# Optimization experiments

Hardware: AMD Instinct MI355X
Metric: run time of the kernel (lower is better)

The kernel has to match this reference:

```python
import jax, jax.numpy as jnp
import numpy as np

DIM = 1024
HEADS = 16
HEAD_DIM = DIM // HEADS
DFF = 4 * DIM  # SwiGLU expansion=4.0
EPS = 1e-5
NEG = -1e4  # original uses -1e4 causal mask, not -inf


def rms_norm(x, w):
    v = jnp.mean(x * x, axis=-1, keepdims=True)
    return w * (x * jax.lax.rsqrt(v + EPS))


def rotate_half(x):
    x1, x2 = jnp.split(x, 2, axis=-1)
    return jnp.concatenate((-x2, x1), axis=-1)


def setup_inputs() -> dict:
    key = jax.random.key(0)
    ks = jax.random.split(key, 12)
    B, S = 2, 2048
    s = 0.02
    h = jax.random.normal(ks[0], (B, S, DIM), jnp.float32)
    # RoPE tables, half-split convention: emb = concat(freqs, freqs)
    inv_freq = 1.0 / (10000.0 ** (np.arange(0, HEAD_DIM, 2, dtype=np.float32) / HEAD_DIM))
    freqs = np.arange(S, dtype=np.float32)[:, None] * inv_freq[None, :]
    emb = np.concatenate([freqs, freqs], axis=-1)
    cos = jnp.asarray(np.cos(emb))  # [S, HEAD_DIM]
    sin = jnp.asarray(np.sin(emb))
    return {
        "h": h, "cos": cos, "sin": sin,
        "norm1_w": jnp.ones((DIM,), jnp.float32),
        "wq": jax.random.normal(ks[1], (DIM, DIM), jnp.float32) * s,
        "wk": jax.random.normal(ks[2], (DIM, DIM), jnp.float32) * s,
        "wv": jax.random.normal(ks[3], (DIM, DIM), jnp.float32) * s,
        "wo": jax.random.normal(ks[4], (DIM, DIM), jnp.float32) * s,
        "norm2_w": jnp.ones((DIM,), jnp.float32),
        "gate_w": jax.random.normal(ks[5], (DFF, DIM), jnp.float32) * s,
        "gate_b": jnp.zeros((DFF,), jnp.float32),
        "up_w": jax.random.normal(ks[6], (DFF, DIM), jnp.float32) * s,
        "up_b": jnp.zeros((DFF,), jnp.float32),
        "down_w": jax.random.normal(ks[7], (DIM, DFF), jnp.float32) * s,
        "down_b": jnp.zeros((DIM,), jnp.float32),
        "gate": jnp.full((DIM,), 0.5, jnp.float32),
    }


def reference(h, cos, sin, norm1_w, wq, wk, wv, wo, norm2_w,
              gate_w, gate_b, up_w, up_b, down_w, down_b, gate):
    B, S, _ = h.shape
    scale = HEAD_DIM ** -0.5

    x = rms_norm(h, norm1_w)

    def heads(t):  # [B,S,DIM] -> [B,H,S,D]
        return t.reshape(B, S, HEADS, HEAD_DIM).transpose(0, 2, 1, 3)

    q = heads(x @ wq.T)
    k = heads(x @ wk.T)
    v = heads(x @ wv.T)

    # inline RoPE (cos/sin broadcast [S,D] over [B,H,S,D])
    q = q * cos + rotate_half(q) * sin
    k = k * cos + rotate_half(k) * sin

    scores = jnp.einsum('bhsd,bhtd->bhst', q, k) * scale
    causal = jnp.triu(jnp.full((S, S), NEG, jnp.float32), k=1)
    scores = scores + causal
    attn = jax.nn.softmax(scores, axis=-1)
    out = jnp.einsum('bhst,bhtd->bhsd', attn, v)
    out = out.transpose(0, 2, 1, 3).reshape(B, S, DIM)
    attn_out = out @ wo.T

    h = h + attn_out

    x2 = rms_norm(h, norm2_w)
    g = jax.nn.silu(x2 @ gate_w.T + gate_b)
    u = x2 @ up_w.T + up_b
    mlp = (g * u) @ down_w.T + down_b

    h = h + jax.nn.sigmoid(gate) * mlp
    return h
```

## Files before the change

kernel.cpp:

```cpp
#include <hip/hip_runtime.h>
#include <math.h>

#define DIM    1024
#define HEADS  16
#define HD     64
#define SEQ    2048
#define BATCH  2
#define TTOK   4096
#define DFF    4096
#define S3     3072

typedef __attribute__((ext_vector_type(8))) short short8;
typedef __attribute__((ext_vector_type(4))) float f32x4;

__device__ __forceinline__ float bf2f(unsigned short u) {
  union { unsigned int u; float f; } v; v.u = ((unsigned int)u) << 16; return v.f;
}
__device__ __forceinline__ unsigned short f2bf(float f) {
  union { float f; unsigned int u; } v; v.f = f;
  return (unsigned short)((v.u + 0x7FFFu + ((v.u >> 16) & 1u)) >> 16);
}
__device__ __forceinline__ unsigned short f2bf_trunc(float f) {
  union { float f; unsigned int u; } v; v.f = f;
  return (unsigned short)(v.u >> 16);
}

#define AS1(p) ((const __attribute__((address_space(1))) void*)(p))
#define AS3(p) ((__attribute__((address_space(3))) void*)(p))

__global__ __launch_bounds__(256) void conv4_k(
    const float* __restrict__ src, unsigned short* __restrict__ dst, int n4)
{
  const int i = blockIdx.x * 256 + threadIdx.x;
  if (i >= n4) return;
  const float4 f = ((const float4*)src)[i];
  unsigned long long o = (unsigned long long)f2bf(f.x)
                       | ((unsigned long long)f2bf(f.y) << 16)
                       | ((unsigned long long)f2bf(f.z) << 32)
                       | ((unsigned long long)f2bf(f.w) << 48);
  ((unsigned long long*)dst)[i] = o;
}

template<int MODE>
__global__ __launch_bounds__(256) void gemm_bt(
    const unsigned short* __restrict__ A,
    const unsigned short* __restrict__ W,
    unsigned short* __restrict__ C,
    float* __restrict__ Cf,
    const float* __restrict__ bias,
    const float* __restrict__ resf,
    const float* __restrict__ gate,
    const float* __restrict__ cosp,
    const float* __restrict__ sinp,
    int M, int N, int K)
{
  __shared__ __align__(16) unsigned short As[128 * 64];
  __shared__ __align__(16) unsigned short Bs[128 * 64];

  const int tid  = threadIdx.x;
  const int lane = tid & 63;
  const int wv   = tid >> 6;
  const int row0 = blockIdx.x * 128;
  const int col0 = blockIdx.y * 128;
  const int wm   = (wv >> 1) * 64;
  const int wn   = (wv & 1) * 64;
  const int lr   = lane & 15;
  const int lg   = lane >> 4;

  const int srow = lane >> 3;
  const int skg  = (lane & 7) ^ srow;

  f32x4 acc[4][4];
#pragma unroll
  for (int i = 0; i < 4; i++)
#pragma unroll
    for (int j = 0; j < 4; j++) acc[i][j] = (f32x4){0.f, 0.f, 0.f, 0.f};

  for (int k0 = 0; k0 < K; k0 += 64) {
#pragma unroll
    for (int i = 0; i < 4; i++) {
      const int c = wv * 4 + i;
      const unsigned short* ga = A + (size_t)(row0 + c * 8 + srow) * K + k0 + skg * 8;
      __builtin_amdgcn_global_load_lds(AS1(ga), AS3(As + c * 512), 16, 0, 0);
      const unsigned short* gb = W + (size_t)(col0 + c * 8 + srow) * K + k0 + skg * 8;
      __builtin_amdgcn_global_load_lds(AS1(gb), AS3(Bs + c * 512), 16, 0, 0);
    }
    __syncthreads();

#pragma unroll
    for (int ks = 0; ks < 2; ks++) {
      short8 af[4], bf[4];
#pragma unroll
      for (int i = 0; i < 4; i++) {
        const int r = wm + i * 16 + lr;
        af[i] = *(const short8*)(As + r * 64 + (((ks * 4 + lg) ^ (lr & 7)) * 8));
      }
#pragma unroll
      for (int j = 0; j < 4; j++) {
        const int r = wn + j * 16 + lr;
        bf[j] = *(const short8*)(Bs + r * 64 + (((ks * 4 + lg) ^ (lr & 7)) * 8));
      }
#pragma unroll
      for (int i = 0; i < 4; i++)
#pragma unroll
        for (int j = 0; j < 4; j++)
          acc[i][j] = __builtin_amdgcn_mfma_f32_16x16x32_bf16(af[i], bf[j], acc[i][j], 0, 0, 0);
    }
    __syncthreads();
  }

  if (MODE == 5) {
    const bool do_rope = (col0 < 2048);
#pragma unroll
    for (int i = 0; i < 4; i++) {
#pragma unroll
      for (int r = 0; r < 4; r++) {
        const int row = row0 + wm + i * 16 + lg * 4 + r;
        const int s = row & (SEQ - 1);
        const size_t rb = (size_t)row * N + col0 + wn;
        if (do_rope) {
#pragma unroll
          for (int jp = 0; jp < 2; jp++) {
            const int d = jp * 16 + lr;
            const float c = cosp[s * HD + d];
            const float sn = sinp[s * HD + d];
            const float x1v = acc[i][jp][r];
            const float x2v = acc[i][jp + 2][r];
            C[rb + d]      = f2bf(x1v * c - x2v * sn);
            C[rb + d + 32] = f2bf(x2v * c + x1v * sn);
          }
        } else {
#pragma unroll
          for (int j = 0; j < 4; j++)
            C[rb + j * 16 + lr] = f2bf(acc[i][j][r]);
        }
      }
    }
    return;
  }

#pragma unroll
  for (int i = 0; i < 4; i++) {
#pragma unroll
    for (int j = 0; j < 4; j++) {
      const int col = col0 + wn + j * 16 + lr;
#pragma unroll
      for (int r = 0; r < 4; r++) {
        const int row = row0 + wm + i * 16 + lg * 4 + r;
        float v = acc[i][j][r];
        const size_t idx = (size_t)row * N + col;
        if (MODE == 3) {
          Cf[idx] = v + resf[idx];
        } else if (MODE == 4) {
          const float sg = 1.0f / (1.0f + __expf(-gate[col]));
          Cf[idx] = Cf[idx] + sg * (v + bias[col]);
        }
      }
    }
  }
}

__global__ __launch_bounds__(256) void gemm_swiglu(
    const unsigned short* __restrict__ A,
    const unsigned short* __restrict__ Wg,
    const unsigned short* __restrict__ Wu,
    unsigned short* __restrict__ G,
    const float* __restrict__ gb,
    const float* __restrict__ ub,
    int M, int N, int K)
{
  __shared__ __align__(16) unsigned short As[128 * 64];
  __shared__ __align__(16) unsigned short Gs[128 * 64];
  __shared__ __align__(16) unsigned short Us[128 * 64];

  const int tid  = threadIdx.x;
  const int lane = tid & 63;
  const int wv   = tid >> 6;
  const int row0 = blockIdx.x * 128;
  const int col0 = blockIdx.y * 128;
  const int wm   = (wv >> 1) * 64;
  const int wn   = (wv & 1) * 64;
  const int lr   = lane & 15;
  const int lg   = lane >> 4;

  const int srow = lane >> 3;
  const int skg  = (lane & 7) ^ srow;

  f32x4 ag[4][4], au[4][4];
#pragma unroll
  for (int i = 0; i < 4; i++)
#pragma unroll
    for (int j = 0; j < 4; j++) {
      ag[i][j] = (f32x4){0.f, 0.f, 0.f, 0.f};
      au[i][j] = (f32x4){0.f, 0.f, 0.f, 0.f};
    }

  for (int k0 = 0; k0 < K; k0 += 64) {
#pragma unroll
    for (int i = 0; i < 4; i++) {
      const int c = wv * 4 + i;
      const unsigned short* ga = A + (size_t)(row0 + c * 8 + srow) * K + k0 + skg * 8;
      __builtin_amdgcn_global_load_lds(AS1(ga), AS3(As + c * 512), 16, 0, 0);
      const unsigned short* gg = Wg + (size_t)(col0 + c * 8 + srow) * K + k0 + skg * 8;
      __builtin_amdgcn_global_load_lds(AS1(gg), AS3(Gs + c * 512), 16, 0, 0);
      const unsigned short* gu = Wu + (size_t)(col0 + c * 8 + srow) * K + k0 + skg * 8;
      __builtin_amdgcn_global_load_lds(AS1(gu), AS3(Us + c * 512), 16, 0, 0);
    }
    __syncthreads();

#pragma unroll
    for (int ks = 0; ks < 2; ks++) {
      short8 af[4], bg[4], bu[4];
#pragma unroll
      for (int i = 0; i < 4; i++) {
        const int r = wm + i * 16 + lr;
        af[i] = *(const short8*)(As + r * 64 + (((ks * 4 + lg) ^ (lr & 7)) * 8));
      }
#pragma unroll
      for (int j = 0; j < 4; j++) {
        const int r = wn + j * 16 + lr;
        const int off = (((ks * 4 + lg) ^ (lr & 7)) * 8);
        bg[j] = *(const short8*)(Gs + r * 64 + off);
        bu[j] = *(const short8*)(Us + r * 64 + off);
      }
#pragma unroll
      for (int i = 0; i < 4; i++)
#pragma unroll
        for (int j = 0; j < 4; j++) {
          ag[i][j] = __builtin_amdgcn_mfma_f32_16x16x32_bf16(af[i], bg[j], ag[i][j], 0, 0, 0);
          au[i][j] = __builtin_amdgcn_mfma_f32_16x16x32_bf16(af[i], bu[j], au[i][j], 0, 0, 0);
        }
    }
    __syncthreads();
  }

#pragma unroll
  for (int i = 0; i < 4; i++) {
#pragma unroll
    for (int j = 0; j < 4; j++) {
      const int col = col0 + wn + j * 16 + lr;
#pragma unroll
      for (int r = 0; r < 4; r++) {
        const int row = row0 + wm + i * 16 + lg * 4 + r;
        float g = ag[i][j][r] + gb[col];
        g = g / (1.0f + __expf(-g));
        const float u = au[i][j][r] + ub[col];
        G[(size_t)row * N + col] = f2bf(g * u);
      }
    }
  }
}

template<int XF32>
__global__ __launch_bounds__(256) void rmsnorm_k(
    const void* __restrict__ Xv,
    const float* __restrict__ W,
    unsigned short* __restrict__ Y)
{
  const int t  = blockIdx.x;
  const int i0 = threadIdx.x * 4;

  float v[4];
  if (XF32) {
    const float4 f = *(const float4*)((const float*)Xv + (size_t)t * DIM + i0);
    v[0] = f.x; v[1] = f.y; v[2] = f.z; v[3] = f.w;
  } else {
    unsigned long long raw = *(const unsigned long long*)((const unsigned short*)Xv + (size_t)t * DIM + i0);
#pragma unroll
    for (int k = 0; k < 4; k++) v[k] = bf2f((unsigned short)(raw >> (16 * k)));
  }

  float ss = v[0] * v[0] + v[1] * v[1] + v[2] * v[2] + v[3] * v[3];
#pragma unroll
  for (int off = 32; off > 0; off >>= 1) ss += __shfl_xor(ss, off);

  __shared__ float red[4];
  if ((threadIdx.x & 63) == 0) red[threadIdx.x >> 6] = ss;
  __syncthreads();
  const float tot = red[0] + red[1] + red[2] + red[3];
  const float r = rsqrtf(tot * (1.0f / DIM) + 1e-5f);

  const float4 wf = *(const float4*)(W + i0);
  const float wv4[4] = {wf.x, wf.y, wf.z, wf.w};
  unsigned long long o = 0;
#pragma unroll
  for (int k = 0; k < 4; k++)
    o |= ((unsigned long long)f2bf(v[k] * r * wv4[k])) << (16 * k);
  *(unsigned long long*)(Y + (size_t)t * DIM + i0) = o;
}

__device__ const unsigned char cqt[24] = {8,9,10,11,12,13,14,15,7,15,6,14,5,13,4,12,3,11,2,10,1,9,0,8};
__device__ const unsigned char cck[24] = {0,0,0,0,0,0,0,0,0,1,0,1,0,1,0,1,0,1,0,1,0,1,0,1};

__global__ __launch_bounds__(256) void fattn_k(
    const unsigned short* __restrict__ QKV,
    unsigned short* __restrict__ O,
    unsigned short* __restrict__ Pbuf,
    float* __restrict__ Lbuf)
{
  __shared__ __align__(16) unsigned short Ks[64 * 64];
  __shared__ __align__(16) unsigned short Vt[64 * 72];
  __shared__ __align__(16) unsigned short Ps[4 * 32 * 72];

  const int tid  = threadIdx.x;
  const int lane = tid & 63;
  const int wv   = tid >> 6;
  const int lr   = lane & 15;
  const int lg   = lane >> 4;

  const int j  = blockIdx.x;
  const int bh = blockIdx.y;
  const int qt = cqt[j];
  const int ck = cck[j];
  const int b  = bh >> 4, h = bh & 15;
  const int q0 = qt * 128;
  const int c0 = ck * 1024;
  const int kend = min(q0 + 128, c0 + 1024);
  const size_t rowb = (size_t)b * SEQ;
  const int qoff = h * HD;
  const int koff = 1024 + h * HD;
  const int voff = 2048 + h * HD;

  short8 aq[2][2];
#pragma unroll
  for (int rf = 0; rf < 2; rf++) {
    const size_t tok = rowb + q0 + wv * 32 + rf * 16 + lr;
    aq[rf][0] = *(const short8*)(QKV + tok * S3 + qoff + lg * 8);
    aq[rf][1] = *(const short8*)(QKV + tok * S3 + qoff + 32 + lg * 8);
  }

  f32x4 o[2][4];
  f32x4 lacc[2];
#pragma unroll
  for (int rf = 0; rf < 2; rf++) {
    lacc[rf] = (f32x4){0.f, 0.f, 0.f, 0.f};
#pragma unroll
    for (int d = 0; d < 4; d++) o[rf][d] = (f32x4){0.f, 0.f, 0.f, 0.f};
  }
  short8 onesb;
#pragma unroll
  for (int jj = 0; jj < 8; jj++) onesb[jj] = (short)0x3F80;

  const int srow = lane >> 3;
  const int skg  = (lane & 7) ^ srow;
  const int kv   = tid >> 2;
  const int d0   = (tid & 3) * 16;

  const float C1 = 0.125f * 1.44269504f;
  const float C2 = 11.5415603f;

  for (int t0 = c0; t0 < kend; t0 += 64) {
#pragma unroll
    for (int i = 0; i < 2; i++) {
      const int c = wv * 2 + i;
      const unsigned short* gk = QKV + (rowb + t0 + c * 8 + srow) * S3 + koff + skg * 8;
      __builtin_amdgcn_global_load_lds(AS1(gk), AS3(Ks + c * 512), 16, 0, 0);
    }
    {
      const unsigned short* gv = QKV + (rowb + t0 + kv) * S3 + voff + d0;
      const short8 v0 = *(const short8*)gv;
      const short8 v1 = *(const short8*)(gv + 8);
      const int klo = kv & 7, khi = kv >> 3;
#pragma unroll
      for (int w = 0; w < 8; w++) {
        const int da = d0 + w, db2 = d0 + 8 + w;
        Vt[da  * 72 + ((khi ^ ((da  >> 3) & 7)) * 8) + klo] = (unsigned short)v0[w];
        Vt[db2 * 72 + ((khi ^ ((db2 >> 3) & 7)) * 8) + klo] = (unsigned short)v1[w];
      }
    }
    __syncthreads();

    f32x4 S[2][4];
#pragma unroll
    for (int sub = 0; sub < 4; sub++) {
      const int kr = sub * 16 + lr;
      const short8 bk0 = *(const short8*)(Ks + kr * 64 + ((lg       ^ (kr & 7)) * 8));
      const short8 bk1 = *(const short8*)(Ks + kr * 64 + (((4 + lg) ^ (kr & 7)) * 8));
#pragma unroll
      for (int rf = 0; rf < 2; rf++) {
        f32x4 s = (f32x4){0.f, 0.f, 0.f, 0.f};
        s = __builtin_amdgcn_mfma_f32_16x16x32_bf16(aq[rf][0], bk0, s, 0, 0, 0);
        s = __builtin_amdgcn_mfma_f32_16x16x32_bf16(aq[rf][1], bk1, s, 0, 0, 0);
        S[rf][sub] = s;
      }
    }

    unsigned short* pw = Ps + wv * (32 * 72);
#pragma unroll
    for (int rf = 0; rf < 2; rf++) {
      const int qmin = q0 + wv * 32 + rf * 16;
      const bool diag = (t0 + 63 > qmin);
#pragma unroll
      for (int sub = 0; sub < 4; sub++) {
#pragma unroll
        for (int r = 0; r < 4; r++) {
          float t = fmaf(S[rf][sub][r], C1, -C2);
          if (diag && (t0 + sub * 16 + lr > qmin + lg * 4 + r)) t = -INFINITY;
          const float p = exp2f(t);
          pw[(rf * 16 + lg * 4 + r) * 72 + sub * 16 + lr] = f2bf_trunc(p);
        }
      }
    }

#pragma unroll
    for (int kf = 0; kf < 2; kf++) {
      const short8 pa0 = *(const short8*)(pw + lr * 72 + kf * 32 + lg * 8);
      const short8 pa1 = *(const short8*)(pw + (16 + lr) * 72 + kf * 32 + lg * 8);
      lacc[0] = __builtin_amdgcn_mfma_f32_16x16x32_bf16(pa0, onesb, lacc[0], 0, 0, 0);
      lacc[1] = __builtin_amdgcn_mfma_f32_16x16x32_bf16(pa1, onesb, lacc[1], 0, 0, 0);
#pragma unroll
      for (int dsub = 0; dsub < 4; dsub++) {
        const int d = dsub * 16 + lr;
        const short8 bvf = *(const short8*)(Vt + d * 72 +
                             (((kf * 4 + lg) ^ ((d >> 3) & 7)) * 8));
        o[0][dsub] = __builtin_amdgcn_mfma_f32_16x16x32_bf16(pa0, bvf, o[0][dsub], 0, 0, 0);
        o[1][dsub] = __builtin_amdgcn_mfma_f32_16x16x32_bf16(pa1, bvf, o[1][dsub], 0, 0, 0);
      }
    }
    __syncthreads();
  }

  if (qt < 8) {
#pragma unroll
    for (int rf = 0; rf < 2; rf++) {
      float inv[4];
#pragma unroll
      for (int r = 0; r < 4; r++) inv[r] = 1.0f / lacc[rf][r];
#pragma unroll
      for (int dsub = 0; dsub < 4; dsub++)
#pragma unroll
        for (int r = 0; r < 4; r++)
          O[(rowb + q0 + wv * 32 + rf * 16 + lg * 4 + r) * DIM + h * HD + dsub * 16 + lr] =
              f2bf(o[rf][dsub][r] * inv[r]);
    }
  } else {
    const int pidx = (bh * 8 + (qt - 8)) * 2 + ck;
    unsigned short* pb = Pbuf + (size_t)pidx * (128 * 64);
    float* lb = Lbuf + pidx * 128;
#pragma unroll
    for (int rf = 0; rf < 2; rf++) {
      const int rbase = wv * 32 + rf * 16 + lg * 4;
      if (lr == 0) {
#pragma unroll
        for (int r = 0; r < 4; r++) lb[rbase + r] = lacc[rf][r];
      }
#pragma unroll
      for (int dsub = 0; dsub < 4; dsub++)
#pragma unroll
        for (int r = 0; r < 4; r++)
          pb[(rbase + r) * 64 + dsub * 16 + lr] = f2bf(o[rf][dsub][r]);
    }
  }
}

__global__ __launch_bounds__(256) void fattn_combine_k(
    const unsigned short* __restrict__ Pbuf,
    const float* __restrict__ Lbuf,
    unsigned short* __restrict__ O)
{
  const int qt = blockIdx.x + 8;
  const int bh = blockIdx.y;
  const int b  = bh >> 4, h = bh & 15;
  const int q0 = qt * 128;
  const size_t rowb = (size_t)b * SEQ;
  const int p0 = (bh * 8 + blockIdx.x) * 2;

  const unsigned short* pa = Pbuf + (size_t)p0 * (128 * 64);
  const unsigned short* pb = pa + 128 * 64;
  const float* la = Lbuf + p0 * 128;
  const float* lb = la + 128;

#pragma unroll
  for (int it = 0; it < 4; it++) {
    const int idx = it * 2048 + threadIdx.x * 8;
    const int row = idx >> 6;
    const int col = idx & 63;
    const short8 v0 = *(const short8*)(pa + idx);
    const short8 v1 = *(const short8*)(pb + idx);
    const float inv = 1.0f / (la[row] + lb[row]);
    short8 r;
#pragma unroll
    for (int w = 0; w < 8; w++)
      r[w] = (short)f2bf((bf2f((unsigned short)v0[w]) + bf2f((unsigned short)v1[w])) * inv);
    *(short8*)(O + (rowb + q0 + row) * DIM + h * HD + col) = r;
  }
}

extern "C" void kernel_launch(void* const* d_in, const int* in_sizes, int n_in,
                              void* d_out, int out_size, void* d_ws, size_t ws_size,
                              hipStream_t stream)
{
  const float* h    = (const float*)d_in[0];
  const float* cosb = (const float*)d_in[1];
  const float* sinb = (const float*)d_in[2];
  const float* n1w  = (const float*)d_in[3];
  const float* n2w  = (const float*)d_in[8];
  const float* gb   = (const float*)d_in[10];
  const float* ub   = (const float*)d_in[12];
  const float* db   = (const float*)d_in[14];
  const float* gatep= (const float*)d_in[15];
  float* out = (float*)d_out;

  unsigned short* ws = (unsigned short*)d_ws;
  const size_t M1 = 1u << 20;

  unsigned short* wqkv = ws;
  unsigned short* wo_c = ws + 3 * M1;
  unsigned short* gw_c = ws + 4 * M1;
  unsigned short* uw_c = ws + 8 * M1;
  unsigned short* dw_c = ws + 12 * M1;
  unsigned short* x1   = ws + 16 * M1;
  unsigned short* Pbuf = ws + 16 * M1;
  unsigned short* x2   = ws + 16 * M1;
  float*          Lbuf = (float*)ws;
  unsigned short* qkv  = ws + 20 * M1;
  unsigned short* attn = ws + 32 * M1;
  unsigned short* g    = qkv;

  const dim3 blk(256);
  const dim3 gq(TTOK / 128, S3 / 128);
  const dim3 g1(TTOK / 128, DIM / 128);
  const dim3 g2(TTOK / 128, DFF / 128);

  auto cv = [&](int i, unsigned short* dst) {
    const int n4 = in_sizes[i] / 4;
    conv4_k<<<(n4 + 255) / 256, blk, 0, stream>>>((const float*)d_in[i], dst, n4);
  };
  cv(4, wqkv); cv(5, wqkv + M1); cv(6, wqkv + 2 * M1); cv(7, wo_c);
  cv(9, gw_c); cv(11, uw_c); cv(13, dw_c);

  rmsnorm_k<1><<<TTOK, blk, 0, stream>>>(h, n1w, x1);

  gemm_bt<5><<<gq, blk, 0, stream>>>(x1, wqkv, qkv, nullptr, nullptr, nullptr,
                                     nullptr, cosb, sinb, TTOK, S3, DIM);

  fattn_k<<<dim3(24, BATCH * HEADS), blk, 0, stream>>>(qkv, attn, Pbuf, Lbuf);
  fattn_combine_k<<<dim3(8, BATCH * HEADS), blk, 0, stream>>>(Pbuf, Lbuf, attn);

  gemm_bt<3><<<g1, blk, 0, stream>>>(attn, wo_c, nullptr, out, nullptr, h,
                                     nullptr, nullptr, nullptr, TTOK, DIM, DIM);

  rmsnorm_k<1><<<TTOK, blk, 0, stream>>>(out, n2w, x2);

  gemm_swiglu<<<g2, blk, 0, stream>>>(x2, gw_c, uw_c, g, gb, ub, TTOK, DFF, DIM);

  gemm_bt<4><<<g1, blk, 0, stream>>>(g, dw_c, nullptr, out, db, nullptr,
                                     gatep, nullptr, nullptr, TTOK, DIM, DFF);
}
```

Measured before the change: 494.5 us.

## Split-K down projection, rebalance causal attention tiles, merge weight conversions, double-buffer KV

Merges the seven weight-conversion launches into one kernel. The down-projection GEMM becomes a 4-way split-K whose bf16 partials are summed by a new combine kernel that also applies bias, sigmoid gate and residual. Flash attention uses a new 32-block schedule that splits long causal query tiles into up to three chunks for load balance, and double-buffers K/V in shared memory so the next tile loads while the current one computes. The aim is better occupancy on the 256-CU device and less launch overhead. The cost is extra partial-sum traffic, a bf16 rounding of partials, and complex hand-coded schedule tables.

After: 465.1 us. 1.06x faster.

```diff
diff --git a/kernel.cpp b/kernel.cpp
--- a/kernel.cpp
+++ b/kernel.cpp
@@ -28,12 +28,21 @@
 #define AS1(p) ((const __attribute__((address_space(1))) void*)(p))
 #define AS3(p) ((__attribute__((address_space(3))) void*)(p))
 
-__global__ __launch_bounds__(256) void conv4_k(
-    const float* __restrict__ src, unsigned short* __restrict__ dst, int n4)
+__global__ __launch_bounds__(256) void wconv_k(
+    const float* __restrict__ s0, const float* __restrict__ s1,
+    const float* __restrict__ s2, const float* __restrict__ s3,
+    const float* __restrict__ s4, const float* __restrict__ s5,
+    const float* __restrict__ s6, unsigned short* __restrict__ dst)
 {
   const int i = blockIdx.x * 256 + threadIdx.x;
-  if (i >= n4) return;
-  const float4 f = ((const float4*)src)[i];
+  const float* s; int base;
+  if (i < 1048576) {
+    if (i < 524288) { if (i < 262144) { s = s0; base = 0; } else { s = s1; base = 262144; } }
+    else            { if (i < 786432) { s = s2; base = 524288; } else { s = s3; base = 786432; } }
+  } else if (i < 2097152) { s = s4; base = 1048576; }
+  else if (i < 3145728)   { s = s5; base = 2097152; }
+  else                    { s = s6; base = 3145728; }
+  const float4 f = ((const float4*)s)[i - base];
   unsigned long long o = (unsigned long long)f2bf(f.x)
                        | ((unsigned long long)f2bf(f.y) << 16)
                        | ((unsigned long long)f2bf(f.z) << 32)
@@ -47,9 +56,7 @@
     const unsigned short* __restrict__ W,
     unsigned short* __restrict__ C,
     float* __restrict__ Cf,
-    const float* __restrict__ bias,
     const float* __restrict__ resf,
-    const float* __restrict__ gate,
     const float* __restrict__ cosp,
     const float* __restrict__ sinp,
     int M, int N, int K)
@@ -70,13 +77,16 @@
   const int srow = lane >> 3;
   const int skg  = (lane & 7) ^ srow;
 
+  int kb = 0, ke = K;
+  if (MODE == 6) { kb = blockIdx.z * 1024; ke = kb + 1024; }
+
   f32x4 acc[4][4];
 #pragma unroll
   for (int i = 0; i < 4; i++)
 #pragma unroll
     for (int j = 0; j < 4; j++) acc[i][j] = (f32x4){0.f, 0.f, 0.f, 0.f};
 
-  for (int k0 = 0; k0 < K; k0 += 64) {
+  for (int k0 = kb; k0 < ke; k0 += 64) {
 #pragma unroll
     for (int i = 0; i < 4; i++) {
       const int c = wv * 4 + i;
@@ -139,6 +149,11 @@
     return;
   }
 
+  unsigned short* Cz = C;
+  if (MODE == 6) {
+    const size_t pz[4] = {4u * 1048576u, 8u * 1048576u, 16u * 1048576u, 0u};
+    Cz = C + pz[blockIdx.z];
+  }
 #pragma unroll
   for (int i = 0; i < 4; i++) {
 #pragma unroll
@@ -147,17 +162,42 @@
 #pragma unroll
       for (int r = 0; r < 4; r++) {
         const int row = row0 + wm + i * 16 + lg * 4 + r;
-        float v = acc[i][j][r];
+        const float v = acc[i][j][r];
         const size_t idx = (size_t)row * N + col;
         if (MODE == 3) {
           Cf[idx] = v + resf[idx];
-        } else if (MODE == 4) {
-          const float sg = 1.0f / (1.0f + __expf(-gate[col]));
-          Cf[idx] = Cf[idx] + sg * (v + bias[col]);
+        } else if (MODE == 6) {
+          Cz[idx] = f2bf(v);
         }
       }
     }
   }
+}
+
+__global__ __launch_bounds__(256) void dcomb_k(
+    const unsigned short* __restrict__ ws, float* __restrict__ out,
+    const float* __restrict__ db, const float* __restrict__ gate)
+{
+  const int i4 = blockIdx.x * 256 + threadIdx.x;
+  const size_t idx = (size_t)i4 * 4;
+  const int col = (int)(idx & 1023);
+  const unsigned long long p0 = *(const unsigned long long*)(ws + 4u * 1048576u + idx);
+  const unsigned long long p1 = *(const unsigned long long*)(ws + 8u * 1048576u + idx);
+  const unsigned long long p2 = *(const unsigned long long*)(ws + 16u * 1048576u + idx);
+  const unsigned long long p3 = *(const unsigned long long*)(ws + idx);
+  float4 o = *(float4*)(out + idx);
+  float* op = (float*)&o;
+#pragma unroll
+  for (int w = 0; w < 4; w++) {
+    const float s = bf2f((unsigned short)(p0 >> (16 * w)))
+                  + bf2f((unsigned short)(p1 >> (16 * w)))
+                  + bf2f((unsigned short)(p2 >> (16 * w)))
+                  + bf2f((unsigned short)(p3 >> (16 * w)))
+                  + db[col + w];
+    const float sg = 1.0f / (1.0f + __expf(-gate[col + w]));
+    op[w] += sg * s;
+  }
+  *(float4*)(out + idx) = o;
 }
 
 __global__ __launch_bounds__(256) void gemm_swiglu(
@@ -289,8 +329,11 @@
   *(unsigned long long*)(Y + (size_t)t * DIM + i0) = o;
 }
 
-__device__ const unsigned char cqt[24] = {8,9,10,11,12,13,14,15,7,15,6,14,5,13,4,12,3,11,2,10,1,9,0,8};
-__device__ const unsigned char cck[24] = {0,0,0,0,0,0,0,0,0,1,0,1,0,1,0,1,0,1,0,1,0,1,0,1};
+__device__ const unsigned char cqt[32] = {10,10,15,15,9,9,13,14,14,14,15,4,8,8,12,12,13,13,7,7,11,11,11,12,3,6,6,5,5,2,1,0};
+__device__ const unsigned char ctb[32] = {0,11,0,11,0,10,0,0,10,20,22,0,0,9,0,9,10,19,0,8,0,8,16,18,0,0,7,0,6,0,0,0};
+__device__ const unsigned char ccnt[32] = {11,11,11,11,10,10,10,10,10,10,10,10,9,9,9,9,9,9,8,8,8,8,8,8,8,7,7,6,6,6,4,2};
+__device__ const unsigned char cchv[32] = {0,1,0,1,0,1,0,0,1,2,2,0,0,1,0,1,1,2,0,1,0,1,2,2,0,0,1,0,1,0,0,0};
+__device__ const unsigned char cpsv[32] = {255,5,255,14,255,4,255,255,12,13,15,255,255,3,255,8,10,11,255,2,255,6,7,9,255,255,1,255,0,255,255,255};
 
 __global__ __launch_bounds__(256) void fattn_k(
     const unsigned short* __restrict__ QKV,
@@ -298,8 +341,8 @@
     unsigned short* __restrict__ Pbuf,
     float* __restrict__ Lbuf)
 {
-  __shared__ __align__(16) unsigned short Ks[64 * 64];
-  __shared__ __align__(16) unsigned short Vt[64 * 72];
+  __shared__ __align__(16) unsigned short Ks[2][64 * 64];
+  __shared__ __align__(16) unsigned short Vt[2][64 * 72];
   __shared__ __align__(16) unsigned short Ps[4 * 32 * 72];
 
   const int tid  = threadIdx.x;
@@ -311,15 +354,16 @@
   const int j  = blockIdx.x;
   const int bh = blockIdx.y;
   const int qt = cqt[j];
-  const int ck = cck[j];
+  const int tb = ctb[j];
+  const int nt = ccnt[j];
+  const int ch = cchv[j];
+  const int ps = cpsv[j];
   const int b  = bh >> 4, h = bh & 15;
   const int q0 = qt * 128;
-  const int c0 = ck * 1024;
-  const int kend = min(q0 + 128, c0 + 1024);
   const size_t rowb = (size_t)b * SEQ;
   const int qoff = h * HD;
-  const int koff = 1024 + h * HD;
-  const int voff = 2048 + h * HD;
+  const int koff = 1024 + qoff;
+  const int voff = 2048 + qoff;
 
   short8 aq[2][2];
 #pragma unroll
@@ -349,33 +393,44 @@
   const float C1 = 0.125f * 1.44269504f;
   const float C2 = 11.5415603f;
 
-  for (int t0 = c0; t0 < kend; t0 += 64) {
+  auto stage = [&](int buf, int ti) {
+    const int t0 = (tb + ti) * 64;
+    unsigned short* ksb = &Ks[buf][0];
 #pragma unroll
     for (int i = 0; i < 2; i++) {
       const int c = wv * 2 + i;
       const unsigned short* gk = QKV + (rowb + t0 + c * 8 + srow) * S3 + koff + skg * 8;
-      __builtin_amdgcn_global_load_lds(AS1(gk), AS3(Ks + c * 512), 16, 0, 0);
-    }
-    {
-      const unsigned short* gv = QKV + (rowb + t0 + kv) * S3 + voff + d0;
-      const short8 v0 = *(const short8*)gv;
-      const short8 v1 = *(const short8*)(gv + 8);
-      const int klo = kv & 7, khi = kv >> 3;
-#pragma unroll
-      for (int w = 0; w < 8; w++) {
-        const int da = d0 + w, db2 = d0 + 8 + w;
-        Vt[da  * 72 + ((khi ^ ((da  >> 3) & 7)) * 8) + klo] = (unsigned short)v0[w];
-        Vt[db2 * 72 + ((khi ^ ((db2 >> 3) & 7)) * 8) + klo] = (unsigned short)v1[w];
-      }
-    }
+      __builtin_amdgcn_global_load_lds(AS1(gk), AS3(ksb + c * 512), 16, 0, 0);
+    }
+    unsigned short* vtb = &Vt[buf][0];
+    const unsigned short* gv = QKV + (rowb + t0 + kv) * S3 + voff + d0;
+    const short8 v0 = *(const short8*)gv;
+    const short8 v1 = *(const short8*)(gv + 8);
+    const int klo = kv & 7, khi = kv >> 3;
+#pragma unroll
+    for (int w = 0; w < 8; w++) {
+      const int da = d0 + w, db2 = d0 + 8 + w;
+      vtb[da  * 72 + ((khi ^ ((da  >> 3) & 7)) * 8) + klo] = (unsigned short)v0[w];
+      vtb[db2 * 72 + ((khi ^ ((db2 >> 3) & 7)) * 8) + klo] = (unsigned short)v1[w];
+    }
+  };
+
+  stage(0, 0);
+
+  for (int ti = 0; ti < nt; ti++) {
     __syncthreads();
+    if (ti + 1 < nt) stage((ti + 1) & 1, ti + 1);
+
+    const int t0 = (tb + ti) * 64;
+    const unsigned short* ksb = &Ks[ti & 1][0];
+    const unsigned short* vtb = &Vt[ti & 1][0];
 
     f32x4 S[2][4];
 #pragma unroll
     for (int sub = 0; sub < 4; sub++) {
       const int kr = sub * 16 + lr;
-      const short8 bk0 = *(const short8*)(Ks + kr * 64 + ((lg       ^ (kr & 7)) * 8));
-      const short8 bk1 = *(const short8*)(Ks + kr * 64 + (((4 + lg) ^ (kr & 7)) * 8));
+      const short8 bk0 = *(const short8*)(ksb + kr * 64 + ((lg       ^ (kr & 7)) * 8));
+      const short8 bk1 = *(const short8*)(ksb + kr * 64 + (((4 + lg) ^ (kr & 7)) * 8));
 #pragma unroll
       for (int rf = 0; rf < 2; rf++) {
         f32x4 s = (f32x4){0.f, 0.f, 0.f, 0.f};
@@ -411,16 +466,15 @@
 #pragma unroll
       for (int dsub = 0; dsub < 4; dsub++) {
         const int d = dsub * 16 + lr;
-        const short8 bvf = *(const short8*)(Vt + d * 72 +
+        const short8 bvf = *(const short8*)(vtb + d * 72 +
                              (((kf * 4 + lg) ^ ((d >> 3) & 7)) * 8));
         o[0][dsub] = __builtin_amdgcn_mfma_f32_16x16x32_bf16(pa0, bvf, o[0][dsub], 0, 0, 0);
         o[1][dsub] = __builtin_amdgcn_mfma_f32_16x16x32_bf16(pa1, bvf, o[1][dsub], 0, 0, 0);
       }
     }
-    __syncthreads();
-  }
-
-  if (qt < 8) {
+  }
+
+  if (ps == 255 && qt < 5) {
 #pragma unroll
     for (int rf = 0; rf < 2; rf++) {
       float inv[4];
@@ -434,21 +488,35 @@
               f2bf(o[rf][dsub][r] * inv[r]);
     }
   } else {
-    const int pidx = (bh * 8 + (qt - 8)) * 2 + ck;
-    unsigned short* pb = Pbuf + (size_t)pidx * (128 * 64);
-    float* lb = Lbuf + pidx * 128;
+    const int lbase = ((bh * 11 + (qt - 5)) * 3 + ch) * 128;
 #pragma unroll
     for (int rf = 0; rf < 2; rf++) {
       const int rbase = wv * 32 + rf * 16 + lg * 4;
       if (lr == 0) {
 #pragma unroll
-        for (int r = 0; r < 4; r++) lb[rbase + r] = lacc[rf][r];
-      }
-#pragma unroll
-      for (int dsub = 0; dsub < 4; dsub++)
-#pragma unroll
-        for (int r = 0; r < 4; r++)
-          pb[(rbase + r) * 64 + dsub * 16 + lr] = f2bf(o[rf][dsub][r]);
+        for (int r = 0; r < 4; r++) Lbuf[lbase + rbase + r] = lacc[rf][r];
+      }
+    }
+    if (ps == 255) {
+#pragma unroll
+      for (int rf = 0; rf < 2; rf++)
+#pragma unroll
+        for (int dsub = 0; dsub < 4; dsub++)
+#pragma unroll
+          for (int r = 0; r < 4; r++)
+            O[(rowb + q0 + wv * 32 + rf * 16 + lg * 4 + r) * DIM + h * HD + dsub * 16 + lr] =
+                f2bf(o[rf][dsub][r]);
+    } else {
+      unsigned short* pb = Pbuf + ((size_t)bh * 16 + ps) * 8192;
+#pragma unroll
+      for (int rf = 0; rf < 2; rf++) {
+        const int rbase = wv * 32 + rf * 16 + lg * 4;
+#pragma unroll
+        for (int dsub = 0; dsub < 4; dsub++)
+#pragma unroll
+          for (int r = 0; r < 4; r++)
+            pb[(rbase + r) * 64 + dsub * 16 + lr] = f2bf(o[rf][dsub][r]);
+      }
     }
   }
 }
@@ -458,31 +526,41 @@
     const float* __restrict__ Lbuf,
     unsigned short* __restrict__ O)
 {
-  const int qt = blockIdx.x + 8;
+  const int qt = 5 + blockIdx.x;
   const int bh = blockIdx.y;
   const int b  = bh >> 4, h = bh & 15;
   const int q0 = qt * 128;
   const size_t rowb = (size_t)b * SEQ;
-  const int p0 = (bh * 8 + blockIdx.x) * 2;
-
-  const unsigned short* pa = Pbuf + (size_t)p0 * (128 * 64);
-  const unsigned short* pb = pa + 128 * 64;
-  const float* la = Lbuf + p0 * 128;
-  const float* lb = la + 128;
+  const int pbase_t[11] = {0, 1, 2, 3, 4, 5, 6, 8, 10, 12, 14};
+  const int pb0 = pbase_t[qt - 5];
+  const int np  = (qt < 11) ? 1 : 2;
+  const int lbase = (bh * 11 + (qt - 5)) * 3 * 128;
+
+  const unsigned short* p0 = Pbuf + ((size_t)bh * 16 + pb0) * 8192;
+  const unsigned short* p1 = Pbuf + ((size_t)bh * 16 + pb0 + 1) * 8192;
 
 #pragma unroll
   for (int it = 0; it < 4; it++) {
     const int idx = it * 2048 + threadIdx.x * 8;
     const int row = idx >> 6;
     const int col = idx & 63;
-    const short8 v0 = *(const short8*)(pa + idx);
-    const short8 v1 = *(const short8*)(pb + idx);
-    const float inv = 1.0f / (la[row] + lb[row]);
+    float ls = Lbuf[lbase + row] + Lbuf[lbase + 128 + row];
+    if (np == 2) ls += Lbuf[lbase + 256 + row];
+    const float inv = 1.0f / ls;
+
+    unsigned short* op = O + (rowb + q0 + row) * DIM + h * HD + col;
+    const short8 vb = *(const short8*)op;
+    const short8 e0 = *(const short8*)(p0 + idx);
+    short8 e1;
+    if (np == 2) e1 = *(const short8*)(p1 + idx);
     short8 r;
 #pragma unroll
-    for (int w = 0; w < 8; w++)
-      r[w] = (short)f2bf((bf2f((unsigned short)v0[w]) + bf2f((unsigned short)v1[w])) * inv);
-    *(short8*)(O + (rowb + q0 + row) * DIM + h * HD + col) = r;
+    for (int w = 0; w < 8; w++) {
+      float s = bf2f((unsigned short)vb[w]) + bf2f((unsigned short)e0[w]);
+      if (np == 2) s += bf2f((unsigned short)e1[w]);
+      r[w] = (short)f2bf(s * inv);
+    }
+    *(short8*)op = r;
   }
 }
 
@@ -521,29 +599,30 @@
   const dim3 gq(TTOK / 128, S3 / 128);
   const dim3 g1(TTOK / 128, DIM / 128);
   const dim3 g2(TTOK / 128, DFF / 128);
-
-  auto cv = [&](int i, unsigned short* dst) {
-    const int n4 = in_sizes[i] / 4;
-    conv4_k<<<(n4 + 255) / 256, blk, 0, stream>>>((const float*)d_in[i], dst, n4);
-  };
-  cv(4, wqkv); cv(5, wqkv + M1); cv(6, wqkv + 2 * M1); cv(7, wo_c);
-  cv(9, gw_c); cv(11, uw_c); cv(13, dw_c);
+  const dim3 gd(TTOK / 128, DIM / 128, 4);
+
+  wconv_k<<<16384, blk, 0, stream>>>(
+      (const float*)d_in[4], (const float*)d_in[5], (const float*)d_in[6],
+      (const float*)d_in[7], (const float*)d_in[9], (const float*)d_in[11],
+      (const float*)d_in[13], ws);
 
   rmsnorm_k<1><<<TTOK, blk, 0, stream>>>(h, n1w, x1);
 
-  gemm_bt<5><<<gq, blk, 0, stream>>>(x1, wqkv, qkv, nullptr, nullptr, nullptr,
-                                     nullptr, cosb, sinb, TTOK, S3, DIM);
-
-  fattn_k<<<dim3(24, BATCH * HEADS), blk, 0, stream>>>(qkv, attn, Pbuf, Lbuf);
-  fattn_combine_k<<<dim3(8, BATCH * HEADS), blk, 0, stream>>>(Pbuf, Lbuf, attn);
-
-  gemm_bt<3><<<g1, blk, 0, stream>>>(attn, wo_c, nullptr, out, nullptr, h,
-                                     nullptr, nullptr, nullptr, TTOK, DIM, DIM);
+  gemm_bt<5><<<gq, blk, 0, stream>>>(x1, wqkv, qkv, nullptr, nullptr,
+                                     cosb, sinb, TTOK, S3, DIM);
+
+  fattn_k<<<dim3(32, BATCH * HEADS), blk, 0, stream>>>(qkv, attn, Pbuf, Lbuf);
+  fattn_combine_k<<<dim3(11, BATCH * HEADS), blk, 0, stream>>>(Pbuf, Lbuf, attn);
+
+  gemm_bt<3><<<g1, blk, 0, stream>>>(attn, wo_c, nullptr, out, h,
+                                     nullptr, nullptr, TTOK, DIM, DIM);
 
   rmsnorm_k<1><<<TTOK, blk, 0, stream>>>(out, n2w, x2);
 
   gemm_swiglu<<<g2, blk, 0, stream>>>(x2, gw_c, uw_c, g, gb, ub, TTOK, DFF, DIM);
 
-  gemm_bt<4><<<g1, blk, 0, stream>>>(g, dw_c, nullptr, out, db, nullptr,
-                                     gatep, nullptr, nullptr, TTOK, DIM, DFF);
-}
+  gemm_bt<6><<<gd, blk, 0, stream>>>(g, dw_c, ws, nullptr, nullptr,
+                                     nullptr, nullptr, TTOK, DIM, DFF);
+
+  dcomb_k<<<4096, blk, 0, stream>>>(ws, out, db, gatep);
+}
```
